# Kernel optimization log

Measured on AMD Instinct MI355X. Metric: run time of the kernel, lower is better.

The kernel has to match this reference:

```python
import jax, jax.numpy as jnp
import numpy as np

HIDDEN = 1024
HEADS = 16
HEAD_DIM = HIDDEN // HEADS  # 64


def setup_inputs() -> dict:
    key = jax.random.key(0)
    ks = jax.random.split(key, 5)
    B, S = 1, 4096
    inputs = jax.random.normal(ks[0], (B, S, HIDDEN), dtype=jnp.float32)
    # Xavier-uniform-ish init for square [out, in] weights (torch Linear layout)
    lim = float(np.sqrt(6.0 / (HIDDEN + HIDDEN)))
    def w(k):
        return jax.random.uniform(k, (HIDDEN, HIDDEN), jnp.float32, -lim, lim)
    return {
        "inputs": inputs,
        "Wq": w(ks[1]), "bq": jnp.zeros((HIDDEN,), jnp.float32),
        "Wk": w(ks[2]), "bk": jnp.zeros((HIDDEN,), jnp.float32),
        "Wv": w(ks[3]), "bv": jnp.zeros((HIDDEN,), jnp.float32),
        "Wo": w(ks[4]), "bo": jnp.zeros((HIDDEN,), jnp.float32),
    }


def reference(inputs, Wq, bq, Wk, bk, Wv, bv, Wo, bo):
    # Chunked online-softmax attention (causal_mask=False) is mathematically
    # identical to standard softmax multi-head attention.
    B, S, _ = inputs.shape
    def proj(W, b):
        # torch Linear: x @ W.T + b, then split heads -> [B, S, H, D]
        return (inputs @ W.T + b).reshape(B, S, HEADS, HEAD_DIM)
    q = proj(Wq, bq) / jnp.asarray(np.sqrt(HEAD_DIM), inputs.dtype)
    k = proj(Wk, bk)
    v = proj(Wv, bv)
    scores = jnp.einsum("bqhd,bkhd->bhqk", q, k)          # [B, H, S, S]
    attn = jax.nn.softmax(scores, axis=-1)
    ctx = jnp.einsum("bhqk,bkhd->bqhd", attn, v)           # [B, S, H, D]
    ctx = ctx.reshape(B, S, HIDDEN)
    return ctx @ Wo.T + bo
```

## Files before the change

kernel.cpp:

```cpp
#include <hip/hip_runtime.h>
#include <hip/hip_bf16.h>

typedef float f32x4 __attribute__((ext_vector_type(4)));
typedef float f32x16 __attribute__((ext_vector_type(16)));
typedef unsigned short u16x8 __attribute__((ext_vector_type(8)));
typedef unsigned int u32x2 __attribute__((ext_vector_type(2)));
typedef unsigned int u32x4 __attribute__((ext_vector_type(4)));
typedef __bf16 b16x8 __attribute__((ext_vector_type(8)));

static __device__ __forceinline__ unsigned short f2bf(float f) {
    unsigned int u = __builtin_bit_cast(unsigned int, f);
    return (unsigned short)((u + 0x7fffu + ((u >> 16) & 1u)) >> 16);
}

static __device__ __forceinline__ unsigned int pkbf(float a, float b) {
    unsigned short x = __builtin_bit_cast(unsigned short, (__bf16)a);
    unsigned short y = __builtin_bit_cast(unsigned short, (__bf16)b);
    return (unsigned int)x | ((unsigned int)y << 16);
}

static __device__ __forceinline__ f32x4 mfma16(u16x8 a, u16x8 b, f32x4 c) {
    return __builtin_amdgcn_mfma_f32_16x16x32_bf16(
        __builtin_bit_cast(b16x8, a), __builtin_bit_cast(b16x8, b), c, 0, 0, 0);
}

static __device__ __forceinline__ f32x16 mfma32(u16x8 a, u16x8 b, f32x16 c) {
    return __builtin_amdgcn_mfma_f32_32x32x16_bf16(
        __builtin_bit_cast(b16x8, a), __builtin_bit_cast(b16x8, b), c, 0, 0, 0);
}

__global__ __launch_bounds__(256)
void convert_x(const float* __restrict__ x, unsigned short* __restrict__ xb)
{
    size_t i = ((size_t)blockIdx.x * 256 + threadIdx.x) * 8;
    f32x4 a = *reinterpret_cast<const f32x4*>(&x[i]);
    f32x4 b = *reinterpret_cast<const f32x4*>(&x[i + 4]);
    u16x8 r;
    r[0] = f2bf(a[0]); r[1] = f2bf(a[1]); r[2] = f2bf(a[2]); r[3] = f2bf(a[3]);
    r[4] = f2bf(b[0]); r[5] = f2bf(b[1]); r[6] = f2bf(b[2]); r[7] = f2bf(b[3]);
    *reinterpret_cast<u16x8*>(&xb[i]) = r;
}

template<bool OUT_F32>
__global__ __launch_bounds__(256)
void gemm_k(const unsigned short* __restrict__ A,
            const float* __restrict__ B0, const float* __restrict__ B1,
            const float* __restrict__ B2,
            const float* __restrict__ bias0, const float* __restrict__ bias1,
            const float* __restrict__ bias2,
            void* c0, void* c1, void* c2,
            int K, float scale0)
{
    __shared__ unsigned short As[128][32];
    __shared__ unsigned short Bs[128][32];
    const int t = (int)threadIdx.x;
    const int wave = t >> 6, lane = t & 63;
    const int wr = wave >> 1, wc = wave & 1;
    const int lo = lane & 15, g = lane >> 4;
    const int brow = blockIdx.y * 128, bcol = blockIdx.x * 128;
    const int w = bcol >> 10;
    const int segcol = bcol & 1023;
    const float* Bw = (w == 0) ? B0 : (w == 1) ? B1 : B2;
    const float* bi = (w == 0) ? bias0 : (w == 1) ? bias1 : bias2;
    const float scale = (w == 0) ? scale0 : 1.0f;

    const int row0 = t >> 2, c8 = t & 3;
    const int row1 = row0 + 64;
    const int brow0 = t >> 3, bc4 = t & 7;

    f32x4 acc[4][4] = {};
    u16x8 aReg[2];
    f32x4 bRegF[4];

    aReg[0] = *reinterpret_cast<const u16x8*>(&A[(size_t)(brow + row0) * K + c8 * 8]);
    aReg[1] = *reinterpret_cast<const u16x8*>(&A[(size_t)(brow + row1) * K + c8 * 8]);
    #pragma unroll
    for (int i = 0; i < 4; ++i)
        bRegF[i] = *reinterpret_cast<const f32x4*>(
            &Bw[(size_t)(segcol + brow0 + i * 32) * K + bc4 * 4]);

    for (int kt = 0; kt < K; kt += 32) {
        __syncthreads();
        *reinterpret_cast<u16x8*>(&As[row0][c8 * 8]) = aReg[0];
        *reinterpret_cast<u16x8*>(&As[row1][c8 * 8]) = aReg[1];
        #pragma unroll
        for (int i = 0; i < 4; ++i) {
            ushort4 u;
            u.x = f2bf(bRegF[i][0]); u.y = f2bf(bRegF[i][1]);
            u.z = f2bf(bRegF[i][2]); u.w = f2bf(bRegF[i][3]);
            *reinterpret_cast<ushort4*>(&Bs[brow0 + i * 32][bc4 * 4]) = u;
        }
        __syncthreads();

        int ktn = kt + 32; if (ktn >= K) ktn = 0;
        aReg[0] = *reinterpret_cast<const u16x8*>(&A[(size_t)(brow + row0) * K + ktn + c8 * 8]);
        aReg[1] = *reinterpret_cast<const u16x8*>(&A[(size_t)(brow + row1) * K + ktn + c8 * 8]);
        #pragma unroll
        for (int i = 0; i < 4; ++i)
            bRegF[i] = *reinterpret_cast<const f32x4*>(
                &Bw[(size_t)(segcol + brow0 + i * 32) * K + ktn + bc4 * 4]);

        u16x8 af[4], bf[4];
        #pragma unroll
        for (int mf = 0; mf < 4; ++mf)
            af[mf] = *reinterpret_cast<const u16x8*>(&As[wr * 64 + mf * 16 + lo][g * 8]);
        #pragma unroll
        for (int nf = 0; nf < 4; ++nf)
            bf[nf] = *reinterpret_cast<const u16x8*>(&Bs[wc * 64 + nf * 16 + lo][g * 8]);
        #pragma unroll
        for (int mf = 0; mf < 4; ++mf)
            #pragma unroll
            for (int nf = 0; nf < 4; ++nf)
                acc[mf][nf] = mfma16(af[mf], bf[nf], acc[mf][nf]);
    }

    void* cp = (w == 0) ? c0 : (w == 1) ? c1 : c2;
    #pragma unroll
    for (int nf = 0; nf < 4; ++nf) {
        int colLocal = wc * 64 + nf * 16 + lo;
        int cw = segcol + colLocal;
        float bv = bi[cw];
        if (w == 2) {
            #pragma unroll
            for (int mf = 0; mf < 4; ++mf) {
                int rowb = brow + wr * 64 + mf * 16 + g * 4;
                ushort4 u;
                u.x = f2bf(acc[mf][nf][0] + bv);
                u.y = f2bf(acc[mf][nf][1] + bv);
                u.z = f2bf(acc[mf][nf][2] + bv);
                u.w = f2bf(acc[mf][nf][3] + bv);
                *reinterpret_cast<ushort4*>(
                    &((unsigned short*)cp)[(size_t)cw * 4096 + rowb]) = u;
            }
        } else {
            #pragma unroll
            for (int mf = 0; mf < 4; ++mf) {
                #pragma unroll
                for (int j = 0; j < 4; ++j) {
                    int row = brow + wr * 64 + mf * 16 + g * 4 + j;
                    float v = (acc[mf][nf][j] + bv) * scale;
                    if constexpr (OUT_F32)
                        ((float*)cp)[(size_t)row * 1024 + cw] = v;
                    else
                        ((unsigned short*)cp)[(size_t)row * 1024 + cw] = f2bf(v);
                }
            }
        }
    }
}

template<int SPLIT>
__global__ __launch_bounds__(256, 2 * SPLIT)
void attn_kernel(const unsigned short* __restrict__ Q,
                 const unsigned short* __restrict__ Kg,
                 const unsigned short* __restrict__ VTg,
                 unsigned short* __restrict__ Ctx,
                 float* __restrict__ Op, float* __restrict__ Lp)
{
    __shared__ unsigned short lds[2][2][4096];
    const int t = (int)threadIdx.x;
    const int lane = t & 63;
    const int q5 = lane & 31;
    const int hi = lane >> 5;
    const int bid = (int)blockIdx.x;
    const int sp = (SPLIT == 2) ? (bid >> 9) : 0;
    const int inner = bid & 511;
    const int h = (inner & 7) | (((inner >> 3) & 1) << 3);
    const int qb = inner >> 4;
    const int hc = h * 64;
    const int wv = t >> 6;
    const int qbase = qb * 128 + wv * 32;
    const int kt0 = sp * (4096 / SPLIT);
    const int NT = 4096 / (SPLIT * 64);

    const int sr = t >> 3, sch = t & 7;
    const int f0 = (sr ^ (sr >> 3)) & 7;
    const int scol0 = (sch ^ f0) * 8;
    const int scol1 = (sch ^ f0 ^ 4) * 8;
    const int sdst = sr * 64 + sch * 8;

    u16x8 qf[4];
    #pragma unroll
    for (int kf = 0; kf < 4; ++kf)
        qf[kf] = *reinterpret_cast<const u16x8*>(
            &Q[(size_t)(qbase + q5) * 1024 + hc + kf * 16 + hi * 8]);

    f32x16 o0 = {}, o1 = {};
    float lsum = 0.f;

    {
        u16x8 k0 = *reinterpret_cast<const u16x8*>(&Kg[(size_t)(kt0 + sr) * 1024 + hc + scol0]);
        u16x8 k1 = *reinterpret_cast<const u16x8*>(&Kg[(size_t)(kt0 + sr + 32) * 1024 + hc + scol1]);
        u16x8 v0 = *reinterpret_cast<const u16x8*>(&VTg[(size_t)(hc + sr) * 4096 + kt0 + scol0]);
        u16x8 v1 = *reinterpret_cast<const u16x8*>(&VTg[(size_t)(hc + sr + 32) * 4096 + kt0 + scol1]);
        *reinterpret_cast<u16x8*>(&lds[0][0][sdst]) = k0;
        *reinterpret_cast<u16x8*>(&lds[0][0][sdst + 2048]) = k1;
        *reinterpret_cast<u16x8*>(&lds[0][1][sdst]) = v0;
        *reinterpret_cast<u16x8*>(&lds[0][1][sdst + 2048]) = v1;
    }

    const int sz0 = (q5 ^ (q5 >> 3)) & 7;
    const int sz1 = sz0 ^ 4;
    int cur = 0;

    for (int tt = 0; tt < NT; ++tt) {
        __syncthreads();

        const int ktn = kt0 + (((tt + 1) & (NT - 1)) << 6);
        u16x8 kn0 = *reinterpret_cast<const u16x8*>(&Kg[(size_t)(ktn + sr) * 1024 + hc + scol0]);
        u16x8 kn1 = *reinterpret_cast<const u16x8*>(&Kg[(size_t)(ktn + sr + 32) * 1024 + hc + scol1]);
        u16x8 vn0 = *reinterpret_cast<const u16x8*>(&VTg[(size_t)(hc + sr) * 4096 + ktn + scol0]);
        u16x8 vn1 = *reinterpret_cast<const u16x8*>(&VTg[(size_t)(hc + sr + 32) * 4096 + ktn + scol1]);

        const unsigned short* Kb = lds[cur][0];
        const unsigned short* Vb = lds[cur][1];

        f32x16 s0 = {}, s1 = {};
        #pragma unroll
        for (int kf = 0; kf < 4; ++kf) {
            int off0 = ((kf * 2 + hi) ^ sz0) * 8;
            int off1 = ((kf * 2 + hi) ^ sz1) * 8;
            u16x8 ka0 = *reinterpret_cast<const u16x8*>(&Kb[q5 * 64 + off0]);
            u16x8 ka1 = *reinterpret_cast<const u16x8*>(&Kb[(q5 + 32) * 64 + off1]);
            s0 = mfma32(ka0, qf[kf], s0);
            s1 = mfma32(ka1, qf[kf], s1);
        }

        unsigned int u0[8], u1[8];
        float ps = 0.f;
        #pragma unroll
        for (int r = 0; r < 8; ++r) {
            float e0 = __builtin_amdgcn_exp2f(s0[2 * r]);
            float e1 = __builtin_amdgcn_exp2f(s0[2 * r + 1]);
            float e2 = __builtin_amdgcn_exp2f(s1[2 * r]);
            float e3 = __builtin_amdgcn_exp2f(s1[2 * r + 1]);
            ps += (e0 + e1) + (e2 + e3);
            u0[r] = pkbf(e0, e1);
            u1[r] = pkbf(e2, e3);
        }
        ps += __shfl_xor(ps, 32);
        lsum += ps;

        u16x8 pa[4];
        #pragma unroll
        for (int b = 0; b < 2; ++b) {
            #pragma unroll
            for (int ks = 0; ks < 2; ++ks) {
                unsigned int x0 = b ? u1[4 * ks]     : u0[4 * ks];
                unsigned int x1 = b ? u1[4 * ks + 1] : u0[4 * ks + 1];
                unsigned int y0 = b ? u1[4 * ks + 2] : u0[4 * ks + 2];
                unsigned int y1 = b ? u1[4 * ks + 3] : u0[4 * ks + 3];
                u32x2 r0 = __builtin_amdgcn_permlane32_swap(x0, y0, false, false);
                u32x2 r1 = __builtin_amdgcn_permlane32_swap(x1, y1, false, false);
                u32x4 d;
                d[0] = r0[0]; d[1] = r1[0]; d[2] = r0[1]; d[3] = r1[1];
                pa[2 * b + ks] = __builtin_bit_cast(u16x8, d);
            }
        }

        #pragma unroll
        for (int ks = 0; ks < 4; ++ks) {
            int off0 = ((ks * 2 + hi) ^ sz0) * 8;
            int off1 = ((ks * 2 + hi) ^ sz1) * 8;
            u16x8 vb0 = *reinterpret_cast<const u16x8*>(&Vb[q5 * 64 + off0]);
            u16x8 vb1 = *reinterpret_cast<const u16x8*>(&Vb[(q5 + 32) * 64 + off1]);
            o0 = mfma32(pa[ks], vb0, o0);
            o1 = mfma32(pa[ks], vb1, o1);
        }

        unsigned short* Kw = lds[cur ^ 1][0];
        unsigned short* Vw = lds[cur ^ 1][1];
        *reinterpret_cast<u16x8*>(&Kw[sdst]) = kn0;
        *reinterpret_cast<u16x8*>(&Kw[sdst + 2048]) = kn1;
        *reinterpret_cast<u16x8*>(&Vw[sdst]) = vn0;
        *reinterpret_cast<u16x8*>(&Vw[sdst + 2048]) = vn1;
        cur ^= 1;
    }

    if constexpr (SPLIT == 1) {
        float linv = 1.f / lsum;
        #pragma unroll
        for (int r = 0; r < 16; ++r) {
            int qr = (r & 3) + 8 * (r >> 2) + 4 * hi;
            float lr = __shfl(linv, qr);
            size_t row = (size_t)(qbase + qr) * 1024 + hc;
            Ctx[row + q5]      = f2bf(o0[r] * lr);
            Ctx[row + 32 + q5] = f2bf(o1[r] * lr);
        }
    } else {
        const int pb = (sp << 9) + (h * 32 + qb);
        float* op = Op + ((size_t)pb * 128 + wv * 32) * 64;
        #pragma unroll
        for (int r = 0; r < 16; ++r) {
            int qr = (r & 3) + 8 * (r >> 2) + 4 * hi;
            op[(size_t)qr * 64 + q5]      = o0[r];
            op[(size_t)qr * 64 + 32 + q5] = o1[r];
        }
        if (hi == 0)
            Lp[(size_t)pb * 128 + wv * 32 + q5] = lsum;
    }
}

__global__ __launch_bounds__(256)
void combine(const float* __restrict__ Op, const float* __restrict__ Lp,
             unsigned short* __restrict__ Ctx)
{
    const int b = (int)blockIdx.x;
    const int h = b >> 5, qb = b & 31;
    const int t = (int)threadIdx.x;
    const int r = t >> 1, dh = (t & 1) * 32;
    const size_t i0 = ((size_t)b * 128 + r) * 64 + dh;
    const size_t i1 = ((size_t)(512 + b) * 128 + r) * 64 + dh;
    const float l = Lp[(size_t)b * 128 + r] + Lp[(size_t)(512 + b) * 128 + r];
    const float inv = 1.f / l;
    const int row = qb * 128 + r;
    unsigned short* dst = &Ctx[(size_t)row * 1024 + h * 64 + dh];
    #pragma unroll
    for (int d = 0; d < 32; d += 8) {
        f32x4 a0 = *reinterpret_cast<const f32x4*>(&Op[i0 + d]);
        f32x4 a1 = *reinterpret_cast<const f32x4*>(&Op[i0 + d + 4]);
        f32x4 b0 = *reinterpret_cast<const f32x4*>(&Op[i1 + d]);
        f32x4 b1 = *reinterpret_cast<const f32x4*>(&Op[i1 + d + 4]);
        u16x8 o;
        #pragma unroll
        for (int j = 0; j < 4; ++j) {
            o[j]     = f2bf((a0[j] + b0[j]) * inv);
            o[4 + j] = f2bf((a1[j] + b1[j]) * inv);
        }
        *reinterpret_cast<u16x8*>(&dst[d]) = o;
    }
}

extern "C" void kernel_launch(void* const* d_in, const int* in_sizes, int n_in,
                              void* d_out, int out_size, void* d_ws, size_t ws_size,
                              hipStream_t stream)
{
    const float* x  = (const float*)d_in[0];
    const float* Wq = (const float*)d_in[1];
    const float* bq = (const float*)d_in[2];
    const float* Wk = (const float*)d_in[3];
    const float* bk = (const float*)d_in[4];
    const float* Wv = (const float*)d_in[5];
    const float* bv = (const float*)d_in[6];
    const float* Wo = (const float*)d_in[7];
    const float* bo = (const float*)d_in[8];
    float* out = (float*)d_out;

    const int S = 4096, HID = 1024;
    const size_t MB = 1u << 20;
    unsigned short* xb  = (unsigned short*)d_ws;
    unsigned short* qws = xb + (size_t)S * HID;
    unsigned short* kws = qws + (size_t)S * HID;
    unsigned short* vtw = kws + (size_t)S * HID;
    unsigned short* cws = xb;
    float* Op = (float*)((char*)d_ws + 32 * MB);
    float* Lp = (float*)((char*)d_ws + 64 * MB);

    const float qscale = 0.125f * 1.44269504088896f;

    convert_x<<<2048, 256, 0, stream>>>(x, xb);

    dim3 gq(24, 32), go(8, 32);
    gemm_k<false><<<gq, 256, 0, stream>>>(xb, Wq, Wk, Wv, bq, bk, bv,
                                          qws, kws, vtw, HID, qscale);

    if (ws_size >= 65 * MB) {
        attn_kernel<2><<<1024, 256, 0, stream>>>(qws, kws, vtw, cws, Op, Lp);
        combine<<<512, 256, 0, stream>>>(Op, Lp, cws);
    } else {
        attn_kernel<1><<<512, 256, 0, stream>>>(qws, kws, vtw, cws, Op, Lp);
    }

    gemm_k<true><<<go, 256, 0, stream>>>(cws, Wo, Wo, Wo, bo, bo, bo,
                                         out, out, out, HID, 1.0f);
}
```

Measured before the change: 179.7 us.

## Pre-convert weights to bf16 and stage tiles via direct global-to-LDS loads

Converts all four weight matrices to bf16 alongside the input in one conversion kernel, so the GEMMs load bf16 tiles instead of converting fp32 inside the K loop. GEMM and attention tile staging switch to global_load_lds asynchronous copies that write straight into shared memory, removing register round-trips. MFMA sections are wrapped with s_setprio to favour matrix work. The GEMM loses its register-level prefetch, so load latency may be exposed there, and the weight conversion adds extra traffic every call.

```diff
diff --git a/kernel.cpp b/kernel.cpp
--- a/kernel.cpp
+++ b/kernel.cpp
@@ -29,23 +29,45 @@
         __builtin_bit_cast(b16x8, a), __builtin_bit_cast(b16x8, b), c, 0, 0, 0);
 }
 
+static __device__ __forceinline__ void gload16(const void* g, void* l) {
+    __builtin_amdgcn_global_load_lds(
+        (const __attribute__((address_space(1))) void*)g,
+        (__attribute__((address_space(3))) void*)l, 16, 0, 0);
+}
+
 __global__ __launch_bounds__(256)
-void convert_x(const float* __restrict__ x, unsigned short* __restrict__ xb)
+void convert_all(const float* __restrict__ x,
+                 const float* __restrict__ wq, const float* __restrict__ wk,
+                 const float* __restrict__ wv, const float* __restrict__ wo,
+                 unsigned short* __restrict__ xb,
+                 unsigned short* __restrict__ wqb, unsigned short* __restrict__ wkb,
+                 unsigned short* __restrict__ wvb, unsigned short* __restrict__ wob)
 {
-    size_t i = ((size_t)blockIdx.x * 256 + threadIdx.x) * 8;
-    f32x4 a = *reinterpret_cast<const f32x4*>(&x[i]);
-    f32x4 b = *reinterpret_cast<const f32x4*>(&x[i + 4]);
+    const int bk = (int)blockIdx.x;
+    const float* src;
+    unsigned short* dst;
+    int base;
+    if (bk < 2048) { src = x; dst = xb; base = bk; }
+    else {
+        int wi = (bk - 2048) >> 9;
+        src = (wi == 0) ? wq : (wi == 1) ? wk : (wi == 2) ? wv : wo;
+        dst = (wi == 0) ? wqb : (wi == 1) ? wkb : (wi == 2) ? wvb : wob;
+        base = (bk - 2048) & 511;
+    }
+    size_t i = ((size_t)base * 256 + threadIdx.x) * 8;
+    f32x4 a = *reinterpret_cast<const f32x4*>(&src[i]);
+    f32x4 b = *reinterpret_cast<const f32x4*>(&src[i + 4]);
     u16x8 r;
     r[0] = f2bf(a[0]); r[1] = f2bf(a[1]); r[2] = f2bf(a[2]); r[3] = f2bf(a[3]);
     r[4] = f2bf(b[0]); r[5] = f2bf(b[1]); r[6] = f2bf(b[2]); r[7] = f2bf(b[3]);
-    *reinterpret_cast<u16x8*>(&xb[i]) = r;
-}
-
-template<bool OUT_F32>
+    *reinterpret_cast<u16x8*>(&dst[i]) = r;
+}
+
+template<bool OUT_F32, bool B_BF16>
 __global__ __launch_bounds__(256)
 void gemm_k(const unsigned short* __restrict__ A,
-            const float* __restrict__ B0, const float* __restrict__ B1,
-            const float* __restrict__ B2,
+            const void* __restrict__ B0v, const void* __restrict__ B1v,
+            const void* __restrict__ B2v,
             const float* __restrict__ bias0, const float* __restrict__ bias1,
             const float* __restrict__ bias2,
             void* c0, void* c1, void* c2,
@@ -60,45 +82,41 @@
     const int brow = blockIdx.y * 128, bcol = blockIdx.x * 128;
     const int w = bcol >> 10;
     const int segcol = bcol & 1023;
-    const float* Bw = (w == 0) ? B0 : (w == 1) ? B1 : B2;
+    const void* Bwv = (w == 0) ? B0v : (w == 1) ? B1v : B2v;
     const float* bi = (w == 0) ? bias0 : (w == 1) ? bias1 : bias2;
     const float scale = (w == 0) ? scale0 : 1.0f;
 
-    const int row0 = t >> 2, c8 = t & 3;
-    const int row1 = row0 + 64;
+    const int glr = lane >> 2, glc = (lane & 3) * 8;
     const int brow0 = t >> 3, bc4 = t & 7;
 
     f32x4 acc[4][4] = {};
-    u16x8 aReg[2];
-    f32x4 bRegF[4];
-
-    aReg[0] = *reinterpret_cast<const u16x8*>(&A[(size_t)(brow + row0) * K + c8 * 8]);
-    aReg[1] = *reinterpret_cast<const u16x8*>(&A[(size_t)(brow + row1) * K + c8 * 8]);
-    #pragma unroll
-    for (int i = 0; i < 4; ++i)
-        bRegF[i] = *reinterpret_cast<const f32x4*>(
-            &Bw[(size_t)(segcol + brow0 + i * 32) * K + bc4 * 4]);
 
     for (int kt = 0; kt < K; kt += 32) {
         __syncthreads();
-        *reinterpret_cast<u16x8*>(&As[row0][c8 * 8]) = aReg[0];
-        *reinterpret_cast<u16x8*>(&As[row1][c8 * 8]) = aReg[1];
-        #pragma unroll
-        for (int i = 0; i < 4; ++i) {
-            ushort4 u;
-            u.x = f2bf(bRegF[i][0]); u.y = f2bf(bRegF[i][1]);
-            u.z = f2bf(bRegF[i][2]); u.w = f2bf(bRegF[i][3]);
-            *reinterpret_cast<ushort4*>(&Bs[brow0 + i * 32][bc4 * 4]) = u;
+        #pragma unroll
+        for (int i = 0; i < 2; ++i) {
+            int r = wave * 32 + i * 16;
+            gload16(&A[(size_t)(brow + r + glr) * K + kt + glc], &As[r][0]);
+        }
+        if constexpr (B_BF16) {
+            const unsigned short* Bp = (const unsigned short*)Bwv;
+            #pragma unroll
+            for (int i = 0; i < 2; ++i) {
+                int r = wave * 32 + i * 16;
+                gload16(&Bp[(size_t)(segcol + r + glr) * K + kt + glc], &Bs[r][0]);
+            }
+        } else {
+            const float* Bp = (const float*)Bwv;
+            #pragma unroll
+            for (int i = 0; i < 4; ++i) {
+                f32x4 v = *reinterpret_cast<const f32x4*>(
+                    &Bp[(size_t)(segcol + brow0 + i * 32) * K + kt + bc4 * 4]);
+                ushort4 u;
+                u.x = f2bf(v[0]); u.y = f2bf(v[1]); u.z = f2bf(v[2]); u.w = f2bf(v[3]);
+                *reinterpret_cast<ushort4*>(&Bs[brow0 + i * 32][bc4 * 4]) = u;
+            }
         }
         __syncthreads();
-
-        int ktn = kt + 32; if (ktn >= K) ktn = 0;
-        aReg[0] = *reinterpret_cast<const u16x8*>(&A[(size_t)(brow + row0) * K + ktn + c8 * 8]);
-        aReg[1] = *reinterpret_cast<const u16x8*>(&A[(size_t)(brow + row1) * K + ktn + c8 * 8]);
-        #pragma unroll
-        for (int i = 0; i < 4; ++i)
-            bRegF[i] = *reinterpret_cast<const f32x4*>(
-                &Bw[(size_t)(segcol + brow0 + i * 32) * K + ktn + bc4 * 4]);
 
         u16x8 af[4], bf[4];
         #pragma unroll
@@ -107,11 +125,13 @@
         #pragma unroll
         for (int nf = 0; nf < 4; ++nf)
             bf[nf] = *reinterpret_cast<const u16x8*>(&Bs[wc * 64 + nf * 16 + lo][g * 8]);
+        __builtin_amdgcn_s_setprio(1);
         #pragma unroll
         for (int mf = 0; mf < 4; ++mf)
             #pragma unroll
             for (int nf = 0; nf < 4; ++nf)
                 acc[mf][nf] = mfma16(af[mf], bf[nf], acc[mf][nf]);
+        __builtin_amdgcn_s_setprio(0);
     }
 
     void* cp = (w == 0) ? c0 : (w == 1) ? c1 : c2;
@@ -173,11 +193,15 @@
     const int kt0 = sp * (4096 / SPLIT);
     const int NT = 4096 / (SPLIT * 64);
 
-    const int sr = t >> 3, sch = t & 7;
-    const int f0 = (sr ^ (sr >> 3)) & 7;
-    const int scol0 = (sch ^ f0) * 8;
-    const int scol1 = (sch ^ f0 ^ 4) * 8;
-    const int sdst = sr * 64 + sch * 8;
+    int kOff[2], vOff[2], lbase[2];
+    #pragma unroll
+    for (int i = 0; i < 2; ++i) {
+        int r = wv * 16 + i * 8 + (lane >> 3);
+        int gc = ((lane & 7) ^ ((r ^ (r >> 3)) & 7)) * 8;
+        kOff[i] = r * 1024 + hc + gc;
+        vOff[i] = (hc + r) * 4096 + gc;
+        lbase[i] = (wv * 16 + i * 8) * 64;
+    }
 
     u16x8 qf[4];
     #pragma unroll
@@ -188,15 +212,10 @@
     f32x16 o0 = {}, o1 = {};
     float lsum = 0.f;
 
-    {
-        u16x8 k0 = *reinterpret_cast<const u16x8*>(&Kg[(size_t)(kt0 + sr) * 1024 + hc + scol0]);
-        u16x8 k1 = *reinterpret_cast<const u16x8*>(&Kg[(size_t)(kt0 + sr + 32) * 1024 + hc + scol1]);
-        u16x8 v0 = *reinterpret_cast<const u16x8*>(&VTg[(size_t)(hc + sr) * 4096 + kt0 + scol0]);
-        u16x8 v1 = *reinterpret_cast<const u16x8*>(&VTg[(size_t)(hc + sr + 32) * 4096 + kt0 + scol1]);
-        *reinterpret_cast<u16x8*>(&lds[0][0][sdst]) = k0;
-        *reinterpret_cast<u16x8*>(&lds[0][0][sdst + 2048]) = k1;
-        *reinterpret_cast<u16x8*>(&lds[0][1][sdst]) = v0;
-        *reinterpret_cast<u16x8*>(&lds[0][1][sdst + 2048]) = v1;
+    #pragma unroll
+    for (int i = 0; i < 2; ++i) {
+        gload16(&Kg[(size_t)kt0 * 1024 + kOff[i]], &lds[0][0][lbase[i]]);
+        gload16(&VTg[(size_t)kt0 + vOff[i]], &lds[0][1][lbase[i]]);
     }
 
     const int sz0 = (q5 ^ (q5 >> 3)) & 7;
@@ -206,16 +225,20 @@
     for (int tt = 0; tt < NT; ++tt) {
         __syncthreads();
 
-        const int ktn = kt0 + (((tt + 1) & (NT - 1)) << 6);
-        u16x8 kn0 = *reinterpret_cast<const u16x8*>(&Kg[(size_t)(ktn + sr) * 1024 + hc + scol0]);
-        u16x8 kn1 = *reinterpret_cast<const u16x8*>(&Kg[(size_t)(ktn + sr + 32) * 1024 + hc + scol1]);
-        u16x8 vn0 = *reinterpret_cast<const u16x8*>(&VTg[(size_t)(hc + sr) * 4096 + ktn + scol0]);
-        u16x8 vn1 = *reinterpret_cast<const u16x8*>(&VTg[(size_t)(hc + sr + 32) * 4096 + ktn + scol1]);
+        if (tt != NT - 1) {
+            const int ktn = kt0 + ((tt + 1) << 6);
+            #pragma unroll
+            for (int i = 0; i < 2; ++i) {
+                gload16(&Kg[(size_t)ktn * 1024 + kOff[i]], &lds[cur ^ 1][0][lbase[i]]);
+                gload16(&VTg[(size_t)ktn + vOff[i]], &lds[cur ^ 1][1][lbase[i]]);
+            }
+        }
 
         const unsigned short* Kb = lds[cur][0];
         const unsigned short* Vb = lds[cur][1];
 
         f32x16 s0 = {}, s1 = {};
+        __builtin_amdgcn_s_setprio(1);
         #pragma unroll
         for (int kf = 0; kf < 4; ++kf) {
             int off0 = ((kf * 2 + hi) ^ sz0) * 8;
@@ -225,6 +248,7 @@
             s0 = mfma32(ka0, qf[kf], s0);
             s1 = mfma32(ka1, qf[kf], s1);
         }
+        __builtin_amdgcn_s_setprio(0);
 
         unsigned int u0[8], u1[8];
         float ps = 0.f;
@@ -258,6 +282,7 @@
             }
         }
 
+        __builtin_amdgcn_s_setprio(1);
         #pragma unroll
         for (int ks = 0; ks < 4; ++ks) {
             int off0 = ((ks * 2 + hi) ^ sz0) * 8;
@@ -267,13 +292,8 @@
             o0 = mfma32(pa[ks], vb0, o0);
             o1 = mfma32(pa[ks], vb1, o1);
         }
-
-        unsigned short* Kw = lds[cur ^ 1][0];
-        unsigned short* Vw = lds[cur ^ 1][1];
-        *reinterpret_cast<u16x8*>(&Kw[sdst]) = kn0;
-        *reinterpret_cast<u16x8*>(&Kw[sdst + 2048]) = kn1;
-        *reinterpret_cast<u16x8*>(&Vw[sdst]) = vn0;
-        *reinterpret_cast<u16x8*>(&Vw[sdst + 2048]) = vn1;
+        __builtin_amdgcn_s_setprio(0);
+
         cur ^= 1;
     }
 
@@ -355,22 +375,39 @@
     unsigned short* cws = xb;
     float* Op = (float*)((char*)d_ws + 32 * MB);
     float* Lp = (float*)((char*)d_ws + 64 * MB);
+    unsigned short* wqb = (unsigned short*)((char*)d_ws + 65 * MB);
+    unsigned short* wkb = wqb + (size_t)HID * HID;
+    unsigned short* wvb = wkb + (size_t)HID * HID;
+    unsigned short* wob = wvb + (size_t)HID * HID;
 
     const float qscale = 0.125f * 1.44269504088896f;
-
-    convert_x<<<2048, 256, 0, stream>>>(x, xb);
+    const bool haveW  = ws_size >= 73 * MB;
+    const bool haveSp = ws_size >= 65 * MB;
+
+    convert_all<<<haveW ? 4096 : 2048, 256, 0, stream>>>(
+        x, Wq, Wk, Wv, Wo, xb, wqb, wkb, wvb, wob);
 
     dim3 gq(24, 32), go(8, 32);
-    gemm_k<false><<<gq, 256, 0, stream>>>(xb, Wq, Wk, Wv, bq, bk, bv,
-                                          qws, kws, vtw, HID, qscale);
-
-    if (ws_size >= 65 * MB) {
+    if (haveW) {
+        gemm_k<false, true><<<gq, 256, 0, stream>>>(xb, wqb, wkb, wvb, bq, bk, bv,
+                                                    qws, kws, vtw, HID, qscale);
+    } else {
+        gemm_k<false, false><<<gq, 256, 0, stream>>>(xb, Wq, Wk, Wv, bq, bk, bv,
+                                                     qws, kws, vtw, HID, qscale);
+    }
+
+    if (haveSp) {
         attn_kernel<2><<<1024, 256, 0, stream>>>(qws, kws, vtw, cws, Op, Lp);
         combine<<<512, 256, 0, stream>>>(Op, Lp, cws);
     } else {
         attn_kernel<1><<<512, 256, 0, stream>>>(qws, kws, vtw, cws, Op, Lp);
     }
 
-    gemm_k<true><<<go, 256, 0, stream>>>(cws, Wo, Wo, Wo, bo, bo, bo,
-                                         out, out, out, HID, 1.0f);
-}
+    if (haveW) {
+        gemm_k<true, true><<<go, 256, 0, stream>>>(cws, wob, wob, wob, bo, bo, bo,
+                                                   out, out, out, HID, 1.0f);
+    } else {
+        gemm_k<true, false><<<go, 256, 0, stream>>>(cws, Wo, Wo, Wo, bo, bo, bo,
+                                                    out, out, out, HID, 1.0f);
+    }
+}
```

Result: slower. 188.0 us (+4.7%).

## Pre-convert weights to bf16 in side kernels and swizzle GEMM block order

Applied to the files above, without the earlier changes.

Weight matrices Wq/Wk/Wv are now converted to bf16 in the same pass that converts x, and Wo is converted inside the combine kernel. The GEMMs therefore load bf16 B tiles directly, halving B traffic and removing per-tile conversion. The QKV GEMM also uses a 1D grid with a grouped block-index swizzle for better L2 reuse. The fallback path for small workspace is removed, so the code now assumes at least 65 MB of workspace.

```diff
diff --git a/kernel.cpp b/kernel.cpp
--- a/kernel.cpp
+++ b/kernel.cpp
@@ -30,22 +30,38 @@
 }
 
 __global__ __launch_bounds__(256)
-void convert_x(const float* __restrict__ x, unsigned short* __restrict__ xb)
+void convert_all(const float* __restrict__ x,
+                 const float* __restrict__ wq, const float* __restrict__ wk,
+                 const float* __restrict__ wv,
+                 unsigned short* __restrict__ xb,
+                 unsigned short* __restrict__ wqb, unsigned short* __restrict__ wkb,
+                 unsigned short* __restrict__ wvb)
 {
-    size_t i = ((size_t)blockIdx.x * 256 + threadIdx.x) * 8;
-    f32x4 a = *reinterpret_cast<const f32x4*>(&x[i]);
-    f32x4 b = *reinterpret_cast<const f32x4*>(&x[i + 4]);
+    const int bk = (int)blockIdx.x;
+    const float* src;
+    unsigned short* dst;
+    int base;
+    if (bk < 2048) { src = x; dst = xb; base = bk; }
+    else {
+        int wi = (bk - 2048) >> 9;
+        src = (wi == 0) ? wq : (wi == 1) ? wk : wv;
+        dst = (wi == 0) ? wqb : (wi == 1) ? wkb : wvb;
+        base = (bk - 2048) & 511;
+    }
+    size_t i = ((size_t)base * 256 + threadIdx.x) * 8;
+    f32x4 a = *reinterpret_cast<const f32x4*>(&src[i]);
+    f32x4 b = *reinterpret_cast<const f32x4*>(&src[i + 4]);
     u16x8 r;
     r[0] = f2bf(a[0]); r[1] = f2bf(a[1]); r[2] = f2bf(a[2]); r[3] = f2bf(a[3]);
     r[4] = f2bf(b[0]); r[5] = f2bf(b[1]); r[6] = f2bf(b[2]); r[7] = f2bf(b[3]);
-    *reinterpret_cast<u16x8*>(&xb[i]) = r;
-}
-
-template<bool OUT_F32>
+    *reinterpret_cast<u16x8*>(&dst[i]) = r;
+}
+
+template<bool OUT_F32, int MODE>
 __global__ __launch_bounds__(256)
 void gemm_k(const unsigned short* __restrict__ A,
-            const float* __restrict__ B0, const float* __restrict__ B1,
-            const float* __restrict__ B2,
+            const unsigned short* __restrict__ B0, const unsigned short* __restrict__ B1,
+            const unsigned short* __restrict__ B2,
             const float* __restrict__ bias0, const float* __restrict__ bias1,
             const float* __restrict__ bias2,
             void* c0, void* c1, void* c2,
@@ -57,48 +73,47 @@
     const int wave = t >> 6, lane = t & 63;
     const int wr = wave >> 1, wc = wave & 1;
     const int lo = lane & 15, g = lane >> 4;
-    const int brow = blockIdx.y * 128, bcol = blockIdx.x * 128;
+
+    const int bid = (int)blockIdx.x;
+    int rowb, colb;
+    if constexpr (MODE == 0) {
+        const int x = bid & 7, c = bid >> 3;
+        rowb = (x >> 1) * 8 + (c & 7);
+        colb = (x & 1) * 12 + (c >> 3);
+    } else {
+        colb = bid & 7; rowb = bid >> 3;
+    }
+    const int brow = rowb * 128, bcol = colb * 128;
     const int w = bcol >> 10;
     const int segcol = bcol & 1023;
-    const float* Bw = (w == 0) ? B0 : (w == 1) ? B1 : B2;
+    const unsigned short* Bw = (w == 0) ? B0 : (w == 1) ? B1 : B2;
     const float* bi = (w == 0) ? bias0 : (w == 1) ? bias1 : bias2;
     const float scale = (w == 0) ? scale0 : 1.0f;
 
     const int row0 = t >> 2, c8 = t & 3;
     const int row1 = row0 + 64;
-    const int brow0 = t >> 3, bc4 = t & 7;
 
     f32x4 acc[4][4] = {};
-    u16x8 aReg[2];
-    f32x4 bRegF[4];
+    u16x8 aReg[2], bReg[2];
 
     aReg[0] = *reinterpret_cast<const u16x8*>(&A[(size_t)(brow + row0) * K + c8 * 8]);
     aReg[1] = *reinterpret_cast<const u16x8*>(&A[(size_t)(brow + row1) * K + c8 * 8]);
-    #pragma unroll
-    for (int i = 0; i < 4; ++i)
-        bRegF[i] = *reinterpret_cast<const f32x4*>(
-            &Bw[(size_t)(segcol + brow0 + i * 32) * K + bc4 * 4]);
+    bReg[0] = *reinterpret_cast<const u16x8*>(&Bw[(size_t)(segcol + row0) * K + c8 * 8]);
+    bReg[1] = *reinterpret_cast<const u16x8*>(&Bw[(size_t)(segcol + row1) * K + c8 * 8]);
 
     for (int kt = 0; kt < K; kt += 32) {
         __syncthreads();
         *reinterpret_cast<u16x8*>(&As[row0][c8 * 8]) = aReg[0];
         *reinterpret_cast<u16x8*>(&As[row1][c8 * 8]) = aReg[1];
-        #pragma unroll
-        for (int i = 0; i < 4; ++i) {
-            ushort4 u;
-            u.x = f2bf(bRegF[i][0]); u.y = f2bf(bRegF[i][1]);
-            u.z = f2bf(bRegF[i][2]); u.w = f2bf(bRegF[i][3]);
-            *reinterpret_cast<ushort4*>(&Bs[brow0 + i * 32][bc4 * 4]) = u;
-        }
+        *reinterpret_cast<u16x8*>(&Bs[row0][c8 * 8]) = bReg[0];
+        *reinterpret_cast<u16x8*>(&Bs[row1][c8 * 8]) = bReg[1];
         __syncthreads();
 
         int ktn = kt + 32; if (ktn >= K) ktn = 0;
         aReg[0] = *reinterpret_cast<const u16x8*>(&A[(size_t)(brow + row0) * K + ktn + c8 * 8]);
         aReg[1] = *reinterpret_cast<const u16x8*>(&A[(size_t)(brow + row1) * K + ktn + c8 * 8]);
-        #pragma unroll
-        for (int i = 0; i < 4; ++i)
-            bRegF[i] = *reinterpret_cast<const f32x4*>(
-                &Bw[(size_t)(segcol + brow0 + i * 32) * K + ktn + bc4 * 4]);
+        bReg[0] = *reinterpret_cast<const u16x8*>(&Bw[(size_t)(segcol + row0) * K + ktn + c8 * 8]);
+        bReg[1] = *reinterpret_cast<const u16x8*>(&Bw[(size_t)(segcol + row1) * K + ktn + c8 * 8]);
 
         u16x8 af[4], bf[4];
         #pragma unroll
@@ -120,17 +135,17 @@
         int colLocal = wc * 64 + nf * 16 + lo;
         int cw = segcol + colLocal;
         float bv = bi[cw];
-        if (w == 2) {
+        if (MODE == 0 && w == 2) {
             #pragma unroll
             for (int mf = 0; mf < 4; ++mf) {
-                int rowb = brow + wr * 64 + mf * 16 + g * 4;
+                int rowb2 = brow + wr * 64 + mf * 16 + g * 4;
                 ushort4 u;
                 u.x = f2bf(acc[mf][nf][0] + bv);
                 u.y = f2bf(acc[mf][nf][1] + bv);
                 u.z = f2bf(acc[mf][nf][2] + bv);
                 u.w = f2bf(acc[mf][nf][3] + bv);
                 *reinterpret_cast<ushort4*>(
-                    &((unsigned short*)cp)[(size_t)cw * 4096 + rowb]) = u;
+                    &((unsigned short*)cp)[(size_t)cw * 4096 + rowb2]) = u;
             }
         } else {
             #pragma unroll
@@ -302,12 +317,24 @@
 }
 
 __global__ __launch_bounds__(256)
-void combine(const float* __restrict__ Op, const float* __restrict__ Lp,
-             unsigned short* __restrict__ Ctx)
+void combine2(const float* __restrict__ Op, const float* __restrict__ Lp,
+              unsigned short* __restrict__ Ctx,
+              const float* __restrict__ Wo, unsigned short* __restrict__ wob)
 {
-    const int b = (int)blockIdx.x;
+    const int bk = (int)blockIdx.x;
+    const int t = (int)threadIdx.x;
+    if (bk >= 512) {
+        size_t i = ((size_t)(bk - 512) * 256 + t) * 8;
+        f32x4 a = *reinterpret_cast<const f32x4*>(&Wo[i]);
+        f32x4 b = *reinterpret_cast<const f32x4*>(&Wo[i + 4]);
+        u16x8 r;
+        r[0] = f2bf(a[0]); r[1] = f2bf(a[1]); r[2] = f2bf(a[2]); r[3] = f2bf(a[3]);
+        r[4] = f2bf(b[0]); r[5] = f2bf(b[1]); r[6] = f2bf(b[2]); r[7] = f2bf(b[3]);
+        *reinterpret_cast<u16x8*>(&wob[i]) = r;
+        return;
+    }
+    const int b = bk;
     const int h = b >> 5, qb = b & 31;
-    const int t = (int)threadIdx.x;
     const int r = t >> 1, dh = (t & 1) * 32;
     const size_t i0 = ((size_t)b * 128 + r) * 64 + dh;
     const size_t i1 = ((size_t)(512 + b) * 128 + r) * 64 + dh;
@@ -355,22 +382,22 @@
     unsigned short* cws = xb;
     float* Op = (float*)((char*)d_ws + 32 * MB);
     float* Lp = (float*)((char*)d_ws + 64 * MB);
+    unsigned short* wqb = (unsigned short*)((char*)d_ws + 32 * MB);
+    unsigned short* wkb = wqb + (size_t)HID * HID;
+    unsigned short* wvb = wkb + (size_t)HID * HID;
+    unsigned short* wob = qws;
 
     const float qscale = 0.125f * 1.44269504088896f;
 
-    convert_x<<<2048, 256, 0, stream>>>(x, xb);
-
-    dim3 gq(24, 32), go(8, 32);
-    gemm_k<false><<<gq, 256, 0, stream>>>(xb, Wq, Wk, Wv, bq, bk, bv,
-                                          qws, kws, vtw, HID, qscale);
-
-    if (ws_size >= 65 * MB) {
-        attn_kernel<2><<<1024, 256, 0, stream>>>(qws, kws, vtw, cws, Op, Lp);
-        combine<<<512, 256, 0, stream>>>(Op, Lp, cws);
-    } else {
-        attn_kernel<1><<<512, 256, 0, stream>>>(qws, kws, vtw, cws, Op, Lp);
-    }
-
-    gemm_k<true><<<go, 256, 0, stream>>>(cws, Wo, Wo, Wo, bo, bo, bo,
-                                         out, out, out, HID, 1.0f);
-}
+    convert_all<<<3584, 256, 0, stream>>>(x, Wq, Wk, Wv, xb, wqb, wkb, wvb);
+
+    gemm_k<false, 0><<<768, 256, 0, stream>>>(xb, wqb, wkb, wvb, bq, bk, bv,
+                                              qws, kws, vtw, HID, qscale);
+
+    attn_kernel<2><<<1024, 256, 0, stream>>>(qws, kws, vtw, cws, Op, Lp);
+
+    combine2<<<1024, 256, 0, stream>>>(Op, Lp, cws, Wo, wob);
+
+    gemm_k<true, 1><<<256, 256, 0, stream>>>(cws, wob, wob, wob, bo, bo, bo,
+                                             out, out, out, HID, 1.0f);
+}
```

New measurement: 175.8 us. 1.02x faster.
